# Kernel optimization log

Hardware: AMD Instinct MI355X
Metric: run time of the kernel (lower is better)

The kernel has to match this reference:

```python
import jax, jax.numpy as jnp
import numpy as np

B, S, HID = 2, 2048, 2048
H, KV, D, E = 16, 4, 128, 32
NB = 9  # num_behavior + 1
EPS = 1e-6
SCALING = (E + D) ** -0.5


def rmsnorm(x, w, eps=EPS):
    # normalize over last dim in fp32, like Qwen3MoeRMSNorm
    xf = x.astype(jnp.float32)
    var = jnp.mean(xf * xf, axis=-1, keepdims=True)
    return (xf * jax.lax.rsqrt(var + eps)).astype(x.dtype) * w


def setup_inputs() -> dict:
    key = jax.random.key(0)
    ks = jax.random.split(key, 12)
    s = lambda n: 1.0 / np.sqrt(n)
    return {
        "hidden_states": jax.random.normal(ks[0], (B, S, HID), jnp.float32),
        "behavior_index": jax.random.randint(ks[1], (B, S), 0, NB),
        "q_proj_w": jax.random.normal(ks[2], (H * D, HID), jnp.float32) * s(HID),
        "k_proj_w": jax.random.normal(ks[3], (KV * D, HID), jnp.float32) * s(HID),
        "v_proj_w": jax.random.normal(ks[4], (KV * D, HID), jnp.float32) * s(HID),
        "o_proj_w": jax.random.normal(ks[5], (HID, H * D), jnp.float32) * s(H * D),
        "q_norm_w": jnp.ones((D,), jnp.float32),
        "k_norm_w": jnp.ones((D,), jnp.float32),
        "qbe_table": jax.random.normal(ks[6], (NB, H * E), jnp.float32),
        "kbe_table": jax.random.normal(ks[7], (NB, KV * E), jnp.float32),
        "qbn_w": jnp.ones((E,), jnp.float32),
        "kbn_w": jnp.ones((E,), jnp.float32),
    }


def reference(hidden_states, behavior_index, q_proj_w, k_proj_w, v_proj_w,
              o_proj_w, q_norm_w, k_norm_w, qbe_table, kbe_table, qbn_w, kbn_w):
    b, s, _ = hidden_states.shape
    # QKV projections + per-head RMSNorm on q/k
    q = rmsnorm((hidden_states @ q_proj_w.T).reshape(b, s, H, D), q_norm_w)
    k = rmsnorm((hidden_states @ k_proj_w.T).reshape(b, s, KV, D), k_norm_w)
    v = (hidden_states @ v_proj_w.T).reshape(b, s, KV, D)
    q = q.transpose(0, 2, 1, 3)  # [b,H,s,D]
    k = k.transpose(0, 2, 1, 3)  # [b,KV,s,D]
    v = v.transpose(0, 2, 1, 3)  # [b,KV,s,D]
    # behavior embeddings: lookup -> per-head RMSNorm -> concat onto head_dim
    qbe = rmsnorm(qbe_table[behavior_index].reshape(b, s, H, E), qbn_w).transpose(0, 2, 1, 3)
    kbe = rmsnorm(kbe_table[behavior_index].reshape(b, s, KV, E), kbn_w).transpose(0, 2, 1, 3)
    q = jnp.concatenate([q, qbe], axis=-1)  # [b,H,s,D+E]
    k = jnp.concatenate([k, kbe], axis=-1)  # [b,KV,s,D+E]
    # GQA: repeat kv heads
    g = H // KV
    k = jnp.repeat(k, g, axis=1)
    v = jnp.repeat(v, g, axis=1)
    # eager attention, causal, softmax in fp32
    scores = jnp.einsum('bhqd,bhkd->bhqk', q, k) * SCALING
    causal = jnp.tril(jnp.ones((s, s), bool))
    scores = jnp.where(causal, scores, jnp.finfo(scores.dtype).min)
    attn = jax.nn.softmax(scores.astype(jnp.float32), axis=-1).astype(q.dtype)
    out = jnp.einsum('bhqk,bhkd->bhqd', attn, v)  # [b,H,s,D]
    out = out.transpose(0, 2, 1, 3).reshape(b, s, H * D)
    return out @ o_proj_w.T
```

## Files before the change

kernel.cpp:

```cpp
#include <hip/hip_runtime.h>

typedef unsigned short u16;
typedef unsigned int u32;
typedef __bf16 bf16x8 __attribute__((ext_vector_type(8)));
typedef __bf16 b16x4 __attribute__((ext_vector_type(4)));
typedef short s16x4 __attribute__((ext_vector_type(4)));
typedef float f32x4 __attribute__((ext_vector_type(4)));

#define SCALE 0.07905694150420949f

__device__ __forceinline__ float bf2f(u16 h) { return __uint_as_float(((u32)h) << 16); }
__device__ __forceinline__ u16 f2bf(float f) {
  u32 u = __float_as_uint(f);
  u += 0x7fffu + ((u >> 16) & 1u);
  return (u16)(u >> 16);
}
__device__ __forceinline__ u16 f2bf_fast(float f) {
  return (u16)((__float_as_uint(f) + 0x8000u) >> 16);
}
__device__ __forceinline__ bf16x8 ldfrag(const u16* p) {
  int4 t = *reinterpret_cast<const int4*>(p);
  return __builtin_bit_cast(bf16x8, t);
}

__device__ __forceinline__ f32x4 mfma16x16(s16x4 a, s16x4 b, f32x4 c) {
#if __has_builtin(__builtin_amdgcn_mfma_f32_16x16x16bf16_1k)
  return __builtin_amdgcn_mfma_f32_16x16x16bf16_1k(a, b, c, 0, 0, 0);
#elif __has_builtin(__builtin_amdgcn_mfma_f32_16x16x16_bf16)
  return __builtin_amdgcn_mfma_f32_16x16x16_bf16(__builtin_bit_cast(b16x4, a),
                                                 __builtin_bit_cast(b16x4, b), c, 0, 0, 0);
#else
  asm volatile("s_nop 2\n\tv_mfma_f32_16x16x16_bf16 %0, %1, %2, %0"
               : "+v"(c) : "v"(a), "v"(b));
  return c;
#endif
}

__device__ __forceinline__ void gld16(const u16* g, u16* l) {
  __builtin_amdgcn_global_load_lds((const __attribute__((address_space(1))) u32*)(const void*)g,
                                   (__attribute__((address_space(3))) u32*)(void*)l, 16, 0, 0);
}

__global__ void conv_f32_bf16(const float* __restrict__ in, u16* __restrict__ out, int n) {
  int n4 = n >> 2;
  for (int i = blockIdx.x * blockDim.x + threadIdx.x; i < n4; i += gridDim.x * blockDim.x) {
    float4 v = reinterpret_cast<const float4*>(in)[i];
    ushort4 o = {f2bf(v.x), f2bf(v.y), f2bf(v.z), f2bf(v.w)};
    reinterpret_cast<ushort4*>(out)[i] = o;
  }
}

template <int OUT_BF16>
__global__ __launch_bounds__(256) void gemm_bt(const u16* __restrict__ A,
                                               const u16* __restrict__ Bw,
                                               void* __restrict__ Cv,
                                               int M, int N, int K) {
  __shared__ __align__(16) u16 As[128][64];
  __shared__ __align__(16) u16 Bs[128][64];
  const int tid = threadIdx.x;
  const int nbn = N >> 7;
  const int bm = blockIdx.x / nbn, bn = blockIdx.x % nbn;
  const int row0 = bm << 7, col0 = bn << 7;
  const int lane = tid & 63, w = tid >> 6;
  const int lg = lane >> 4, lr = lane & 15;
  const int wr = w >> 1, wc = w & 1;
  const int wbase = tid & ~63;
  f32x4 acc[4][4] = {};
  for (int k0 = 0; k0 < K; k0 += 64) {
#pragma unroll
    for (int it = 0; it < 4; ++it) {
      int i = it * 256 + tid;
      int r = i >> 3, c = (i & 7) << 3;
      gld16(&A[(size_t)(row0 + r) * K + k0 + c], (u16*)As + (size_t)(it * 256 + wbase) * 8);
      gld16(&Bw[(size_t)(col0 + r) * K + k0 + c], (u16*)Bs + (size_t)(it * 256 + wbase) * 8);
    }
    __syncthreads();
#pragma unroll
    for (int kk = 0; kk < 2; ++kk) {
      bf16x8 af[4], bv[4];
#pragma unroll
      for (int m = 0; m < 4; ++m) af[m] = ldfrag(&As[wr * 64 + m * 16 + lr][kk * 32 + lg * 8]);
#pragma unroll
      for (int n = 0; n < 4; ++n) bv[n] = ldfrag(&Bs[wc * 64 + n * 16 + lr][kk * 32 + lg * 8]);
#pragma unroll
      for (int m = 0; m < 4; ++m)
#pragma unroll
        for (int n = 0; n < 4; ++n)
          acc[m][n] = __builtin_amdgcn_mfma_f32_16x16x32_bf16(af[m], bv[n], acc[m][n], 0, 0, 0);
    }
    __syncthreads();
  }
#pragma unroll
  for (int m = 0; m < 4; ++m)
#pragma unroll
    for (int n = 0; n < 4; ++n)
#pragma unroll
      for (int r = 0; r < 4; ++r) {
        int row = row0 + wr * 64 + m * 16 + lg * 4 + r;
        int col = col0 + wc * 64 + n * 16 + lr;
        float v = acc[m][n][r];
        if (OUT_BF16)
          ((u16*)Cv)[(size_t)row * N + col] = f2bf(v);
        else
          ((float*)Cv)[(size_t)row * N + col] = v;
      }
}

__global__ __launch_bounds__(256) void postproc(
    const u16* __restrict__ qkv, const int* __restrict__ bidx,
    const float* __restrict__ qnw, const float* __restrict__ knw,
    const float* __restrict__ qbe_t, const float* __restrict__ kbe_t,
    const float* __restrict__ qbn, const float* __restrict__ kbn,
    u16* __restrict__ qcat, u16* __restrict__ kcat, u16* __restrict__ vt) {
  const int tok = blockIdx.x;
  const int b = tok >> 11, s = tok & 2047;
  const int w = threadIdx.x >> 6, lane = threadIdx.x & 63;
  const int idx = bidx[tok];
  const u16* base = qkv + (size_t)tok * 3072;

  for (int h = w; h < 16; h += 4) {
    float x0 = bf2f(base[h * 128 + 2 * lane]);
    float x1 = bf2f(base[h * 128 + 2 * lane + 1]);
    float ss = x0 * x0 + x1 * x1;
#pragma unroll
    for (int o = 32; o; o >>= 1) ss += __shfl_xor(ss, o);
    float rn = rsqrtf(ss * (1.f / 128.f) + 1e-6f) * SCALE;
    size_t ob = ((size_t)(b * 16 + h) * 2048 + s) * 160;
    qcat[ob + 2 * lane] = f2bf(x0 * rn * qnw[2 * lane]);
    qcat[ob + 2 * lane + 1] = f2bf(x1 * rn * qnw[2 * lane + 1]);
    if (lane < 32) {
      float e = qbe_t[idx * 512 + h * 32 + lane];
      float s2 = e * e;
#pragma unroll
      for (int o = 16; o; o >>= 1) s2 += __shfl_xor(s2, o);
      qcat[ob + 128 + lane] = f2bf(e * rsqrtf(s2 * (1.f / 32.f) + 1e-6f) * qbn[lane] * SCALE);
    }
  }
  {
    const int kv = w;
    float x0 = bf2f(base[2048 + kv * 128 + 2 * lane]);
    float x1 = bf2f(base[2048 + kv * 128 + 2 * lane + 1]);
    float ss = x0 * x0 + x1 * x1;
#pragma unroll
    for (int o = 32; o; o >>= 1) ss += __shfl_xor(ss, o);
    float rn = rsqrtf(ss * (1.f / 128.f) + 1e-6f);
    size_t ob = ((size_t)(b * 4 + kv) * 2048 + s) * 160;
    kcat[ob + 2 * lane] = f2bf(x0 * rn * knw[2 * lane]);
    kcat[ob + 2 * lane + 1] = f2bf(x1 * rn * knw[2 * lane + 1]);
    if (lane < 32) {
      float e = kbe_t[idx * 128 + kv * 32 + lane];
      float s2 = e * e;
#pragma unroll
      for (int o = 16; o; o >>= 1) s2 += __shfl_xor(s2, o);
      kcat[ob + 128 + lane] = f2bf(e * rsqrtf(s2 * (1.f / 32.f) + 1e-6f) * kbn[lane]);
    }
    size_t vb = (size_t)(b * 4 + kv) * 128 * 2048;
    vt[vb + (size_t)lane * 2048 + s] = base[2560 + kv * 128 + lane];
    vt[vb + (size_t)(lane + 64) * 2048 + s] = base[2560 + kv * 128 + 64 + lane];
  }
}

__global__ __launch_bounds__(256, 2) void attn(const u16* __restrict__ qcat,
                                               const u16* __restrict__ kcat,
                                               const u16* __restrict__ vt,
                                               u16* __restrict__ aout) {
  __shared__ __align__(16) u16 Kls[2][10240];
  __shared__ __align__(16) u16 Vls[8192];
  const int tid = threadIdx.x;
  const int blk = blockIdx.x;
  const int kvh = blk & 3;
  const int b = (blk >> 2) & 1;
  const int hq = (blk >> 3) & 3;
  const int g = blk >> 5;
  const int h = kvh * 4 + hq;
  const int w = tid >> 6;
  const int lane = tid & 63;
  const int lg = lane >> 4, lr = lane & 15;
  const int qb_a = g * 4 + w;
  const int qb_b = 127 - qb_a;
  const int qpa = qb_a * 16 + lr;
  const int qpb = qb_b * 16 + lr;
  const int nt = 32 - g;

  const u16* qpA = qcat + ((size_t)(b * 16 + h) * 2048 + qb_a * 16) * 160;
  const u16* qpB = qcat + ((size_t)(b * 16 + h) * 2048 + qb_b * 16) * 160;
  bf16x8 qfa[5], qfb[5];
#pragma unroll
  for (int c = 0; c < 5; ++c) {
    qfa[c] = ldfrag(qpA + lr * 160 + c * 32 + lg * 8);
    qfb[c] = ldfrag(qpB + lr * 160 + c * 32 + lg * 8);
  }

  const u16* kbp = kcat + (size_t)(b * 4 + kvh) * 2048 * 160;
  const u16* vbp = vt + (size_t)(b * 4 + kvh) * 128 * 2048;

  auto stageK = [&](int buf, int kt) {
    const u16* ksrc = kbp + (size_t)kt * (64 * 160);
#pragma unroll
    for (int it = 0; it < 5; ++it) {
      int G = it * 256 + tid;
      int r = G / 20, p = G - r * 20;
      int gs = p ^ ((r >> 1) & 3);
      gld16(ksrc + r * 160 + gs * 8, &Kls[buf][G * 8]);
    }
  };
  auto stageV = [&](int kt) {
    const u16* vsrc = vbp + kt * 64;
#pragma unroll
    for (int it = 0; it < 4; ++it) {
      int G = it * 256 + tid;
      int r = G >> 3, p = G & 7;
      int gs = p ^ (r & 7);
      gld16(vsrc + (size_t)r * 2048 + gs * 8, &Vls[G * 8]);
    }
  };

  float ma = -INFINITY, la = 0.f, mb = -INFINITY, lb = 0.f;
  f32x4 acc_a[8] = {}, acc_b[8] = {};

  stageK(0, 0);
  stageV(0);
  __syncthreads();

  for (int kt = 0; kt < nt; ++kt) {
    const int buf = kt & 1;
    const bool aact = (kt <= g);
    if (kt + 1 < nt) stageK(buf ^ 1, kt + 1);

    f32x4 sa[4] = {}, sb[4] = {};
#pragma unroll
    for (int c = 0; c < 5; ++c) {
      bf16x8 kf[4];
#pragma unroll
      for (int i = 0; i < 4; ++i) {
        int r = i * 16 + lr;
        int p = (c * 4 + lg) ^ ((r >> 1) & 3);
        kf[i] = ldfrag(&Kls[buf][(r * 20 + p) * 8]);
      }
#pragma unroll
      for (int i = 0; i < 4; ++i)
        sb[i] = __builtin_amdgcn_mfma_f32_16x16x32_bf16(kf[i], qfb[c], sb[i], 0, 0, 0);
      if (aact)
#pragma unroll
        for (int i = 0; i < 4; ++i)
          sa[i] = __builtin_amdgcn_mfma_f32_16x16x32_bf16(kf[i], qfa[c], sa[i], 0, 0, 0);
    }

    s16x4 pka[4], pkb[4];
    auto soft = [&](f32x4 (&st)[4], float& mm, float& ls, f32x4 (&ac)[8], s16x4 (&pk)[4],
                    bool masked, int qpos) {
      float vmax = -INFINITY;
#pragma unroll
      for (int i = 0; i < 4; ++i)
#pragma unroll
        for (int r = 0; r < 4; ++r) {
          float v = st[i][r];
          if (masked && (kt * 64 + i * 16 + 4 * lg + r > qpos)) v = -INFINITY;
          st[i][r] = v;
          vmax = fmaxf(vmax, v);
        }
      vmax = fmaxf(vmax, __shfl_xor(vmax, 16));
      vmax = fmaxf(vmax, __shfl_xor(vmax, 32));
      bool skip = __all(vmax <= mm);
      float mn = skip ? mm : fmaxf(mm, vmax);
      float rs = 0.f;
#pragma unroll
      for (int i = 0; i < 4; ++i)
#pragma unroll
        for (int r = 0; r < 4; ++r) {
          float p = __expf(st[i][r] - mn);
          st[i][r] = p;
          rs += p;
        }
      rs += __shfl_xor(rs, 16);
      rs += __shfl_xor(rs, 32);
      if (skip) {
        ls += rs;
      } else {
        float corr = __expf(mm - mn);
        ls = ls * corr + rs;
        mm = mn;
        float c4[4];
#pragma unroll
        for (int r = 0; r < 4; ++r) c4[r] = __shfl(corr, 4 * lg + r);
#pragma unroll
        for (int dt = 0; dt < 8; ++dt)
#pragma unroll
          for (int r = 0; r < 4; ++r) ac[dt][r] *= c4[r];
      }
#pragma unroll
      for (int i = 0; i < 4; ++i) {
        pk[i][0] = (short)f2bf_fast(st[i][0]);
        pk[i][1] = (short)f2bf_fast(st[i][1]);
        pk[i][2] = (short)f2bf_fast(st[i][2]);
        pk[i][3] = (short)f2bf_fast(st[i][3]);
      }
    };
    soft(sb, mb, lb, acc_b, pkb, kt == nt - 1, qpb);
    if (aact) soft(sa, ma, la, acc_a, pka, kt == g, qpa);

    __syncthreads();

#pragma unroll
    for (int ks = 0; ks < 4; ++ks) {
      s16x4 vf[8];
#pragma unroll
      for (int dt = 0; dt < 8; ++dt) {
        int r = dt * 16 + lr;
        int p = (ks * 2 + (lg >> 1)) ^ (r & 7);
        vf[dt] = *reinterpret_cast<const s16x4*>(&Vls[(r * 8 + p) * 8 + (lg & 1) * 4]);
      }
#pragma unroll
      for (int dt = 0; dt < 8; ++dt) acc_b[dt] = mfma16x16(pkb[ks], vf[dt], acc_b[dt]);
      if (aact)
#pragma unroll
        for (int dt = 0; dt < 8; ++dt) acc_a[dt] = mfma16x16(pka[ks], vf[dt], acc_a[dt]);
    }

    __syncthreads();
    if (kt + 1 < nt) stageV(kt + 1);
  }

  float inva[4], invb[4];
#pragma unroll
  for (int r = 0; r < 4; ++r) {
    inva[r] = 1.f / __shfl(la, 4 * lg + r);
    invb[r] = 1.f / __shfl(lb, 4 * lg + r);
  }
#pragma unroll
  for (int dt = 0; dt < 8; ++dt)
#pragma unroll
    for (int r = 0; r < 4; ++r) {
      int rowa = qb_a * 16 + 4 * lg + r;
      int rowb = qb_b * 16 + 4 * lg + r;
      aout[((size_t)(b * 2048 + rowa) * 16 + h) * 128 + dt * 16 + lr] =
          f2bf(acc_a[dt][r] * inva[r]);
      aout[((size_t)(b * 2048 + rowb) * 16 + h) * 128 + dt * 16 + lr] =
          f2bf(acc_b[dt][r] * invb[r]);
    }
}

extern "C" void kernel_launch(void* const* d_in, const int* in_sizes, int n_in,
                              void* d_out, int out_size, void* d_ws, size_t ws_size,
                              hipStream_t stream) {
  const float* hs = (const float*)d_in[0];
  const int* bidx = (const int*)d_in[1];
  const float* qw = (const float*)d_in[2];
  const float* kw = (const float*)d_in[3];
  const float* vw = (const float*)d_in[4];
  const float* ow = (const float*)d_in[5];
  const float* qnw = (const float*)d_in[6];
  const float* knw = (const float*)d_in[7];
  const float* qbe_t = (const float*)d_in[8];
  const float* kbe_t = (const float*)d_in[9];
  const float* qbn = (const float*)d_in[10];
  const float* kbn = (const float*)d_in[11];

  u16* ws = (u16*)d_ws;
  u16* hs_bf = ws;
  u16* wqkv = hs_bf + 8388608;
  u16* ow_bf = wqkv + 6291456;
  u16* qkv = ow_bf + 4194304;
  u16* qcat = qkv + 12582912;
  u16* kcat = qcat + 10485760;
  u16* vt = kcat + 2621440;
  u16* attn_o = vt + 2097152;

  conv_f32_bf16<<<2048, 256, 0, stream>>>(hs, hs_bf, 8388608);
  conv_f32_bf16<<<1024, 256, 0, stream>>>(qw, wqkv, 4194304);
  conv_f32_bf16<<<512, 256, 0, stream>>>(kw, wqkv + 4194304, 1048576);
  conv_f32_bf16<<<512, 256, 0, stream>>>(vw, wqkv + 5242880, 1048576);
  conv_f32_bf16<<<1024, 256, 0, stream>>>(ow, ow_bf, 4194304);

  gemm_bt<1><<<dim3((4096 / 128) * (3072 / 128)), 256, 0, stream>>>(
      hs_bf, wqkv, (void*)qkv, 4096, 3072, 2048);

  postproc<<<4096, 256, 0, stream>>>(qkv, bidx, qnw, knw, qbe_t, kbe_t, qbn, kbn,
                                     qcat, kcat, vt);

  attn<<<512, 256, 0, stream>>>(qcat, kcat, vt, attn_o);

  gemm_bt<0><<<dim3((4096 / 128) * (2048 / 128)), 256, 0, stream>>>(
      attn_o, ow_bf, (void*)d_out, 4096, 2048, 2048);
}
```

Before: 263.0 us.

## Double-buffer GEMM tiles with XOR-swizzled LDS layout and block swizzle

Restructures the bf16 GEMM so the next K-tile is staged into a second LDS buffer while the current one feeds MFMA, removing one barrier per iteration. It applies an XOR swizzle to the LDS chunk layout to cut bank conflicts on fragment reads, and remaps block indices to improve L2 locality. It also adds a launch bound of two blocks per CU. The cost is doubled LDS per block (64KB), which may limit occupancy. The code also relies on gld16 writing each lane's 16-byte chunk to that lane's own address.

```diff
diff --git a/kernel.cpp b/kernel.cpp
--- a/kernel.cpp
+++ b/kernel.cpp
@@ -51,37 +51,57 @@
 }
 
 template <int OUT_BF16>
-__global__ __launch_bounds__(256) void gemm_bt(const u16* __restrict__ A,
-                                               const u16* __restrict__ Bw,
-                                               void* __restrict__ Cv,
-                                               int M, int N, int K) {
-  __shared__ __align__(16) u16 As[128][64];
-  __shared__ __align__(16) u16 Bs[128][64];
+__global__ __launch_bounds__(256, 2) void gemm_bt(const u16* __restrict__ A,
+                                                  const u16* __restrict__ Bw,
+                                                  void* __restrict__ Cv,
+                                                  int M, int N, int K) {
+  __shared__ __align__(16) u16 As[2][8192];
+  __shared__ __align__(16) u16 Bs[2][8192];
   const int tid = threadIdx.x;
   const int nbn = N >> 7;
-  const int bm = blockIdx.x / nbn, bn = blockIdx.x % nbn;
+  const int cpx = gridDim.x >> 3;
+  const int swz = (blockIdx.x & 7) * cpx + (blockIdx.x >> 3);
+  const int bm = swz / nbn, bn = swz % nbn;
   const int row0 = bm << 7, col0 = bn << 7;
   const int lane = tid & 63, w = tid >> 6;
   const int lg = lane >> 4, lr = lane & 15;
   const int wr = w >> 1, wc = w & 1;
-  const int wbase = tid & ~63;
+  const int nt = K >> 6;
+
+  auto stage = [&](int slot, int t) {
+    const size_t k0 = (size_t)t << 6;
+#pragma unroll
+    for (int it = 0; it < 4; ++it) {
+      int G = it * 256 + tid;
+      int r = G >> 3, p = G & 7;
+      int gs = p ^ (r & 7);
+      gld16(&A[(size_t)(row0 + r) * K + k0 + gs * 8], &As[slot][(size_t)G * 8]);
+      gld16(&Bw[(size_t)(col0 + r) * K + k0 + gs * 8], &Bs[slot][(size_t)G * 8]);
+    }
+  };
+
   f32x4 acc[4][4] = {};
-  for (int k0 = 0; k0 < K; k0 += 64) {
-#pragma unroll
-    for (int it = 0; it < 4; ++it) {
-      int i = it * 256 + tid;
-      int r = i >> 3, c = (i & 7) << 3;
-      gld16(&A[(size_t)(row0 + r) * K + k0 + c], (u16*)As + (size_t)(it * 256 + wbase) * 8);
-      gld16(&Bw[(size_t)(col0 + r) * K + k0 + c], (u16*)Bs + (size_t)(it * 256 + wbase) * 8);
-    }
-    __syncthreads();
+  stage(0, 0);
+  __syncthreads();
+
+  for (int t = 0; t < nt; ++t) {
+    const int slot = t & 1;
+    if (t + 1 < nt) stage(slot ^ 1, t + 1);
 #pragma unroll
     for (int kk = 0; kk < 2; ++kk) {
       bf16x8 af[4], bv[4];
 #pragma unroll
-      for (int m = 0; m < 4; ++m) af[m] = ldfrag(&As[wr * 64 + m * 16 + lr][kk * 32 + lg * 8]);
-#pragma unroll
-      for (int n = 0; n < 4; ++n) bv[n] = ldfrag(&Bs[wc * 64 + n * 16 + lr][kk * 32 + lg * 8]);
+      for (int m = 0; m < 4; ++m) {
+        int r = wr * 64 + m * 16 + lr;
+        int g = (kk * 4 + lg) ^ (lr & 7);
+        af[m] = ldfrag(&As[slot][r * 64 + g * 8]);
+      }
+#pragma unroll
+      for (int n = 0; n < 4; ++n) {
+        int r = wc * 64 + n * 16 + lr;
+        int g = (kk * 4 + lg) ^ (lr & 7);
+        bv[n] = ldfrag(&Bs[slot][r * 64 + g * 8]);
+      }
 #pragma unroll
       for (int m = 0; m < 4; ++m)
 #pragma unroll
@@ -90,6 +110,7 @@
     }
     __syncthreads();
   }
+
 #pragma unroll
   for (int m = 0; m < 4; ++m)
 #pragma unroll
```

Result: faster. 229.8 us (-12.6%).
